# Kernel optimization log

Measured on AMD Instinct MI355X. Metric: run time of the kernel, lower is better.

Reference implementation:

```python
import jax, jax.numpy as jnp
import numpy as np

HASH = 1 << 12
EPS = 1e-5
_OFFS = [(dx, dy, dz) for dx in (-1, 0, 1) for dy in (-1, 0, 1) for dz in (-1, 0, 1)]
_KOFF = [k for k, o in enumerate(_OFFS) if o != (0, 0, 0)]  # 26 non-center taps
_CENTER = 13


def _hkey(c):
    c = c.astype(np.int64)
    return (c[:, 0] * HASH + c[:, 1]) * HASH + c[:, 2]


def _rand_coords(rng, n, R):
    idx = rng.choice(R ** 3, size=n, replace=False)
    return np.stack(np.unravel_index(idx, (R, R, R)), axis=1).astype(np.int64)


def _conv3_maps(coords):
    # ME kernel map for a 3x3x3 stride-1 conv (in coords == out coords):
    # per non-center tap, (gather_idx, scatter_idx) pairs found by hash lookup.
    n = coords.shape[0]
    keys = _hkey(coords)
    order = np.argsort(keys)
    skeys = keys[order]
    ins, outs = [], []
    for k in _KOFF:
        qk = _hkey(coords + np.asarray(_OFFS[k], np.int64))
        pos = np.clip(np.searchsorted(skeys, qk), 0, n - 1)
        valid = skeys[pos] == qk
        outs.append(np.nonzero(valid)[0].astype(np.int32))
        ins.append(order[pos[valid]].astype(np.int32))
    m = max(len(a) for a in ins)
    im = np.zeros((26, m), np.int32)    # pad gathers with row 0
    om = np.full((26, m), n, np.int32)  # pad scatters into scrap row n (dropped)
    for j in range(26):
        im[j, :len(ins[j])] = ins[j]
        om[j, :len(outs[j])] = outs[j]
    return np.stack([im, om])  # [2, 26, M]


def _children(coords):
    # generative transpose conv k=2 s=2 output coords, ordered o*n + i
    offs = np.array([[a, b, c] for a in (0, 1) for b in (0, 1) for c in (0, 1)], np.int64)
    return (2 * coords[None] + offs[:, None]).reshape(-1, 3)


def _union(ca, cb):
    # sparse-tensor addition domain: union of coordinate sets
    ka, kb = _hkey(ca), _hkey(cb)
    ku = np.unique(np.concatenate([ka, kb]))
    cu = np.stack([ku // (HASH * HASH), (ku // HASH) % HASH, ku % HASH], axis=1)
    return cu, np.searchsorted(ku, ka).astype(np.int32), np.searchsorted(ku, kb).astype(np.int32)


def _sconv3(x, W, m):
    # sparse 3^3 conv as gather-GEMM-scatter; center tap is a plain GEMM
    n = x.shape[0]
    acc = jnp.zeros((n + 1, W.shape[2]), x.dtype)
    for j, k in enumerate(_KOFF):
        acc = acc.at[m[1, j]].add(x[m[0, j]] @ W[k])
    return acc[:n] + x @ W[_CENTER]


def _bn_elu(x, p):
    # MinkowskiBatchNorm (training-mode batch stats over active voxels) + ELU
    mu = jnp.mean(x, axis=0)
    var = jnp.mean(jnp.square(x - mu), axis=0)
    return jax.nn.elu(p[0] * (x - mu) * jax.lax.rsqrt(var + EPS) + p[1])


def _up_block(x, Wt, Wc, m, pa, pb):
    # generative transpose conv (every voxel emits 8 children, order o*n+i) -> BN -> ELU -> conv3 -> BN -> ELU
    t = jnp.einsum('nc,ocd->ond', x, Wt).reshape(-1, Wt.shape[2])
    return _bn_elu(_sconv3(_bn_elu(t, pa), Wc, m), pb)


def setup_inputs() -> dict:
    rng = np.random.default_rng(0)
    N2, N1, N0 = 1200, 6000, 16000
    C2 = _rand_coords(rng, N2, 40)
    C1 = _rand_coords(rng, N1, 80)
    C0 = _rand_coords(rng, N0, 160)
    G2 = _children(C2)                       # coords after up_block_2 transpose conv
    U1, lat1_idx, up1_idx = _union(C1, G2)   # inputs[1] + x domain
    G1 = _children(U1)
    U0, lat0_idx, up0_idx = _union(C0, G1)   # inputs[0] + x domain

    key = jax.random.key(0)
    ks = list(jax.random.split(key, 32))
    kit = iter(ks)

    def w(shape, fan_in):
        return jax.random.normal(next(kit), shape, jnp.float32) * np.float32(1.0 / np.sqrt(fan_in))

    def bn(c):
        g = 1.0 + 0.1 * jax.random.normal(next(kit), (c,), jnp.float32)
        b = 0.1 * jax.random.normal(next(kit), (c,), jnp.float32)
        return jnp.stack([g, b])

    return dict(
        feats0=jax.random.normal(next(kit), (N0, 64), jnp.float32),
        feats1=jax.random.normal(next(kit), (N1, 128), jnp.float32),
        feats2=jax.random.normal(next(kit), (N2, 256), jnp.float32),
        w_out0=w((27, 64, 128), 27 * 64),
        w_out1=w((27, 128, 128), 27 * 128),
        w_out2=w((27, 256, 128), 27 * 256),
        wt2=w((8, 256, 128), 256),
        wu2=w((27, 128, 128), 27 * 128),
        wt1=w((8, 128, 64), 128),
        wu1=w((27, 64, 64), 27 * 64),
        bn_out0=bn(128), bn_out1=bn(128), bn_out2=bn(128),
        bn_up2a=bn(128), bn_up2b=bn(128),
        bn_up1a=bn(64), bn_up1b=bn(64),
        u1_base=jnp.zeros((U1.shape[0], 128), jnp.float32),
        u0_base=jnp.zeros((U0.shape[0], 64), jnp.float32),
        m_c2=jnp.asarray(_conv3_maps(C2)),
        m_g2=jnp.asarray(_conv3_maps(G2)),
        m_u1=jnp.asarray(_conv3_maps(U1)),
        m_g1=jnp.asarray(_conv3_maps(G1)),
        m_u0=jnp.asarray(_conv3_maps(U0)),
        lat1_idx=jnp.asarray(lat1_idx), up1_idx=jnp.asarray(up1_idx),
        lat0_idx=jnp.asarray(lat0_idx), up0_idx=jnp.asarray(up0_idx),
    )


def reference(feats0, feats1, feats2, w_out0, w_out1, w_out2, wt2, wu2, wt1, wu1,
              bn_out0, bn_out1, bn_out2, bn_up2a, bn_up2b, bn_up1a, bn_up1b,
              u1_base, u0_base, m_c2, m_g2, m_u1, m_g1, m_u0,
              lat1_idx, up1_idx, lat0_idx, up0_idx):
    # i = 2 (top)
    out2 = _bn_elu(_sconv3(feats2, w_out2, m_c2), bn_out2)
    t = _up_block(feats2, wt2, wu2, m_g2, bn_up2a, bn_up2b)
    # i = 1: sparse add over union of coords, then out/up blocks
    x1 = u1_base.at[lat1_idx].add(feats1).at[up1_idx].add(t)
    out1 = _bn_elu(_sconv3(x1, w_out1, m_u1), bn_out1)
    t = _up_block(x1, wt1, wu1, m_g1, bn_up1a, bn_up1b)
    # i = 0
    x0 = u0_base.at[lat0_idx].add(feats0).at[up0_idx].add(t)
    out0 = _bn_elu(_sconv3(x0, w_out0, m_u0), bn_out0)
    return out0, out1, out2
```

## Files before the change

kernel.cpp:

```cpp
#include <hip/hip_runtime.h>

typedef __bf16 bf16x8 __attribute__((ext_vector_type(8)));
typedef float  f32x4  __attribute__((ext_vector_type(4)));

__device__ __forceinline__ float b2f(unsigned short u) {
    union { unsigned int i; float f; } v; v.i = ((unsigned int)u) << 16; return v.f;
}
__device__ __forceinline__ unsigned short f2b(float f) {
    union { float f; unsigned int i; } v; v.f = f;
    unsigned int u = v.i;
    return (unsigned short)((u + 0x7fffu + ((u >> 16) & 1u)) >> 16);
}

__global__ void table_init(int* __restrict__ tab, int n)
{
    int idx = blockIdx.x * blockDim.x + threadIdx.x;
    if (idx >= n * 27) return;
    tab[idx] = ((idx % 27) == 13) ? (idx / 27) : n;
}

__global__ void table_fill(int* __restrict__ tab, const int* __restrict__ map, int M, int n)
{
    int tid = blockIdx.x * blockDim.x + threadIdx.x;
    if (tid >= 26 * M) return;
    int j = tid / M, q = tid - j * M;
    int om = map[(26 + j) * M + q];
    if (om < n) {
        int k = (j < 13) ? j : j + 1;
        tab[om * 27 + k] = map[j * M + q];
    }
}

__global__ void pack_w(const float* __restrict__ W, unsigned short* __restrict__ P,
                       int total, int log2Cout, int log2KC)
{
    int tid = blockIdx.x * blockDim.x + threadIdx.x;
    if (tid >= total) return;
    int jj   = tid & 7;
    int cout = (tid >> 3) & ((1 << log2Cout) - 1);
    int rest = tid >> (3 + log2Cout);
    int quad = rest & 3;
    int kj   = rest >> 2;
    int kc   = kj & ((1 << log2KC) - 1);
    int j    = kj >> log2KC;
    int Cin  = (1 << log2KC) * 32;
    int Cout = 1 << log2Cout;
    P[tid] = f2b(W[((size_t)j * Cin + kc * 32 + quad * 8 + jj) * Cout + cout]);
}

__global__ void cast_bf16(const float* __restrict__ X, unsigned short* __restrict__ Y, int nElem)
{
    int tid = blockIdx.x * blockDim.x + threadIdx.x;
    if (tid < nElem) Y[tid] = f2b(X[tid]);
}

template<int T, int KC, bool OUTBF16>
__global__ __launch_bounds__(256) void conv_mfma_st(
    const unsigned short* __restrict__ Xb, const unsigned short* __restrict__ P,
    const int* __restrict__ tab, void* __restrict__ OutV, int n, int nblk)
{
    constexpr int Cin = KC * 32, Cout = 64 * T;
    constexpr int STRIDE = KC * 32 + 8;
    constexpr int CHUNKS = KC * 4;
    constexpr int RPR = 256 / CHUNKS;
    __shared__ int tps[64 * 27];
    __shared__ unsigned short abuf[2][64 * STRIDE];

    const int t = threadIdx.x, lane = t & 63, wv = t >> 6;
    const int m = lane & 15, quad = lane >> 4;

    const int q = nblk >> 3, rr = nblk & 7;
    const int xcd = blockIdx.x & 7, pos = blockIdx.x >> 3;
    const int bswz = (xcd < rr) ? (xcd * (q + 1) + pos) : (rr * (q + 1) + (xcd - rr) * q + pos);
    const int r0 = bswz * 64;
    int rows = n - r0; if (rows > 64) rows = 64;

    for (int e = t; e < 64 * 27; e += 256)
        tps[e] = (e < rows * 27) ? tab[(size_t)r0 * 27 + e] : n;
    __syncthreads();

    const int sr = t / CHUNKS;
    const int sc = t % CHUNKS;

    f32x4 acc[4][T];
    #pragma unroll
    for (int rt = 0; rt < 4; rt++)
        #pragma unroll
        for (int c = 0; c < T; c++) acc[rt][c] = f32x4{0.f, 0.f, 0.f, 0.f};

    uint4 sreg[KC];

    #pragma unroll
    for (int rd = 0; rd < KC; rd++) {
        int r = rd * RPR + sr;
        int in = tps[r * 27];
        sreg[rd] = *reinterpret_cast<const uint4*>(Xb + (size_t)in * Cin + sc * 8);
    }
    #pragma unroll
    for (int rd = 0; rd < KC; rd++) {
        int r = rd * RPR + sr;
        *reinterpret_cast<uint4*>(&abuf[0][r * STRIDE + sc * 8]) = sreg[rd];
    }
    __syncthreads();

    for (int j = 0; j < 27; j++) {
        const int cur = j & 1;
        if (j + 1 < 27) {
            #pragma unroll
            for (int rd = 0; rd < KC; rd++) {
                int r = rd * RPR + sr;
                int in = tps[r * 27 + j + 1];
                sreg[rd] = *reinterpret_cast<const uint4*>(Xb + (size_t)in * Cin + sc * 8);
            }
        }
        #pragma unroll
        for (int kc = 0; kc < KC; kc++) {
            bf16x8 a[4];
            #pragma unroll
            for (int rt = 0; rt < 4; rt++)
                a[rt] = *reinterpret_cast<const bf16x8*>(&abuf[cur][(rt * 16 + m) * STRIDE + kc * 32 + quad * 8]);
            const unsigned short* bp = P + ((size_t)((j * KC + kc) * 4 + quad) * Cout + wv * (T * 16)) * 8;
            #pragma unroll
            for (int c = 0; c < T; c++) {
                bf16x8 b = *reinterpret_cast<const bf16x8*>(bp + (c * 16 + m) * 8);
                #pragma unroll
                for (int rt = 0; rt < 4; rt++)
                    acc[rt][c] = __builtin_amdgcn_mfma_f32_16x16x32_bf16(a[rt], b, acc[rt][c], 0, 0, 0);
            }
        }
        if (j + 1 < 27) {
            #pragma unroll
            for (int rd = 0; rd < KC; rd++) {
                int r = rd * RPR + sr;
                *reinterpret_cast<uint4*>(&abuf[cur ^ 1][r * STRIDE + sc * 8]) = sreg[rd];
            }
        }
        __syncthreads();
    }

    #pragma unroll
    for (int c = 0; c < T; c++) {
        int cout = (wv * T + c) * 16 + m;
        #pragma unroll
        for (int rt = 0; rt < 4; rt++) {
            #pragma unroll
            for (int reg = 0; reg < 4; reg++) {
                int r = rt * 16 + quad * 4 + reg;
                if (r < rows) {
                    size_t off = (size_t)(r0 + r) * Cout + cout;
                    if (OUTBF16) ((unsigned short*)OutV)[off] = f2b(acc[rt][c][reg]);
                    else         ((float*)OutV)[off] = acc[rt][c][reg];
                }
            }
        }
    }
}

template<int T, int RB, bool OUTBF16>
__global__ __launch_bounds__(256) void conv_mfma(
    const unsigned short* __restrict__ Xb, const unsigned short* __restrict__ P,
    const int* __restrict__ tab, void* __restrict__ OutV, int n, int Cin, int KC, int nblk)
{
    const int Cout = 64 * T;
    const int ROWS = RB * 16;
    __shared__ int tps[RB * 16 * 27];
    __shared__ int vld[27];
    const int t = threadIdx.x, lane = t & 63, wv = t >> 6;
    const int m = lane & 15, quad = lane >> 4;

    const int q = nblk >> 3, rr = nblk & 7;
    const int xcd = blockIdx.x & 7, pos = blockIdx.x >> 3;
    const int bswz = (xcd < rr) ? (xcd * (q + 1) + pos) : (rr * (q + 1) + (xcd - rr) * q + pos);
    const int r0 = bswz * ROWS;
    int rows = n - r0; if (rows > ROWS) rows = ROWS;

    for (int e = t; e < ROWS * 27; e += 256)
        tps[e] = (e < rows * 27) ? tab[(size_t)r0 * 27 + e] : n;
    __syncthreads();
    if constexpr (RB == 1) {
        if (t < 27) {
            int v = 0;
            for (int r = 0; r < 16; r++) v |= (tps[r * 27 + t] < n) ? 1 : 0;
            vld[t] = v;
        }
        __syncthreads();
    }

    f32x4 acc[RB][T];
    #pragma unroll
    for (int rt = 0; rt < RB; rt++)
        #pragma unroll
        for (int c = 0; c < T; c++) acc[rt][c] = f32x4{0.f, 0.f, 0.f, 0.f};

    const unsigned short* Xq = Xb + quad * 8;
    const unsigned short* Pq = P + ((size_t)quad * Cout + wv * (T * 16)) * 8;

    for (int j = 0; j < 27; j++) {
        if constexpr (RB == 1) {
            if (!vld[j]) continue;
        }
        int in[RB];
        #pragma unroll
        for (int rt = 0; rt < RB; rt++) in[rt] = tps[(rt * 16 + m) * 27 + j];
        for (int kc = 0; kc < KC; kc++) {
            bf16x8 a[RB];
            #pragma unroll
            for (int rt = 0; rt < RB; rt++)
                a[rt] = *reinterpret_cast<const bf16x8*>(Xq + (size_t)in[rt] * Cin + kc * 32);
            const unsigned short* bp = Pq + (size_t)((j * KC + kc) * 4) * Cout * 8;
            #pragma unroll
            for (int c = 0; c < T; c++) {
                bf16x8 b = *reinterpret_cast<const bf16x8*>(bp + (c * 16 + m) * 8);
                #pragma unroll
                for (int rt = 0; rt < RB; rt++)
                    acc[rt][c] = __builtin_amdgcn_mfma_f32_16x16x32_bf16(a[rt], b, acc[rt][c], 0, 0, 0);
            }
        }
    }

    #pragma unroll
    for (int c = 0; c < T; c++) {
        int cout = (wv * T + c) * 16 + m;
        #pragma unroll
        for (int rt = 0; rt < RB; rt++) {
            #pragma unroll
            for (int reg = 0; reg < 4; reg++) {
                int r = rt * 16 + quad * 4 + reg;
                if (r < rows) {
                    size_t off = (size_t)(r0 + r) * Cout + cout;
                    if (OUTBF16) ((unsigned short*)OutV)[off] = f2b(acc[rt][c][reg]);
                    else         ((float*)OutV)[off] = acc[rt][c][reg];
                }
            }
        }
    }
}

template<int KC, int T>
__global__ __launch_bounds__(256) void tconv_mfma(
    const unsigned short* __restrict__ Xb, const unsigned short* __restrict__ P,
    unsigned short* __restrict__ Out, int n)
{
    const int Cin = KC * 32, Cout = 64 * T;
    const int t = threadIdx.x, lane = t & 63, wv = t >> 6;
    const int m = lane & 15, quad = lane >> 4;
    const int r0 = blockIdx.x * 16;
    int rows = n - r0; if (rows > 16) rows = 16;

    bf16x8 a[KC];
    #pragma unroll
    for (int kc = 0; kc < KC; kc++) {
        a[kc] = bf16x8{};
        if (m < rows)
            a[kc] = *reinterpret_cast<const bf16x8*>(Xb + (size_t)(r0 + m) * Cin + kc * 32 + quad * 8);
    }

    for (int o = 0; o < 8; o++) {
        f32x4 acc[T];
        #pragma unroll
        for (int c = 0; c < T; c++) acc[c] = f32x4{0.f, 0.f, 0.f, 0.f};
        #pragma unroll
        for (int kc = 0; kc < KC; kc++) {
            const unsigned short* bp = P + ((size_t)((o * KC + kc) * 4 + quad) * Cout + wv * (T * 16)) * 8;
            #pragma unroll
            for (int c = 0; c < T; c++) {
                bf16x8 b = *reinterpret_cast<const bf16x8*>(bp + (c * 16 + m) * 8);
                acc[c] = __builtin_amdgcn_mfma_f32_16x16x32_bf16(a[kc], b, acc[c], 0, 0, 0);
            }
        }
        #pragma unroll
        for (int c = 0; c < T; c++) {
            int cout = (wv * T + c) * 16 + m;
            #pragma unroll
            for (int reg = 0; reg < 4; reg++) {
                int r = quad * 4 + reg;
                if (r < rows)
                    Out[((size_t)o * n + r0 + r) * Cout + cout] = f2b(acc[c][reg]);
            }
        }
    }
}

__global__ void scatter_add_f32(float* __restrict__ dst, const float* __restrict__ src,
                                const int* __restrict__ idx, long total, int C)
{
    long tid = (long)blockIdx.x * blockDim.x + threadIdx.x;
    if (tid >= total) return;
    long r = tid / C;
    int  c = (int)(tid - r * C);
    dst[(long)idx[r] * C + c] += src[tid];
}

__global__ void scatter_add_b16(float* __restrict__ dst, const unsigned short* __restrict__ src,
                                const int* __restrict__ idx, long total, int C)
{
    long tid = (long)blockIdx.x * blockDim.x + threadIdx.x;
    if (tid >= total) return;
    long r = tid / C;
    int  c = (int)(tid - r * C);
    dst[(long)idx[r] * C + c] += b2f(src[tid]);
}

template<bool BF16>
__global__ void bn_stats_k(const void* __restrict__ Xv, float* __restrict__ stats,
                           int n, int C, int rowsPerBlock)
{
    const int t = threadIdx.x;
    const int c = t & (C - 1);
    const int sub = t / C;
    const int nsub = 256 / C;
    int r0 = blockIdx.x * rowsPerBlock + sub;
    int r1 = blockIdx.x * rowsPerBlock + rowsPerBlock;
    if (r1 > n) r1 = n;
    float s = 0.f, ss = 0.f;
    for (int r = r0; r < r1; r += nsub) {
        float v = BF16 ? b2f(((const unsigned short*)Xv)[(long)r * C + c])
                       : ((const float*)Xv)[(long)r * C + c];
        s += v; ss += v * v;
    }
    __shared__ float bs[256];
    __shared__ float bq[256];
    bs[t] = s; bq[t] = ss;
    __syncthreads();
    if (sub == 0) {
        for (int k = 1; k < nsub; k++) { s += bs[k * C + c]; ss += bq[k * C + c]; }
        atomicAdd(&stats[c], s);
        atomicAdd(&stats[C + c], ss);
    }
}

template<bool BF16>
__global__ void bn_apply_k(void* __restrict__ Xv, const float* __restrict__ stats,
                           const float* __restrict__ gb, long total, int C, float invn)
{
    long tid = (long)blockIdx.x * blockDim.x + threadIdx.x;
    if (tid >= total) return;
    int c = (int)(tid & (C - 1));
    float mu  = stats[c] * invn;
    float var = stats[C + c] * invn - mu * mu;
    float sc  = gb[c] * rsqrtf(var + 1e-5f);
    float x   = BF16 ? b2f(((unsigned short*)Xv)[tid]) : ((float*)Xv)[tid];
    float v   = (x - mu) * sc + gb[C + c];
    v = (v > 0.f) ? v : expm1f(v);
    if (BF16) ((unsigned short*)Xv)[tid] = f2b(v);
    else      ((float*)Xv)[tid] = v;
}

extern "C" void kernel_launch(void* const* d_in, const int* in_sizes, int n_in,
                              void* d_out, int out_size, void* d_ws, size_t ws_size,
                              hipStream_t stream)
{
    const float* feats0  = (const float*)d_in[0];
    const float* feats1  = (const float*)d_in[1];
    const float* feats2  = (const float*)d_in[2];
    const float* w_out0  = (const float*)d_in[3];
    const float* w_out1  = (const float*)d_in[4];
    const float* w_out2  = (const float*)d_in[5];
    const float* wt2     = (const float*)d_in[6];
    const float* wu2     = (const float*)d_in[7];
    const float* wt1     = (const float*)d_in[8];
    const float* wu1     = (const float*)d_in[9];
    const float* bn_out0 = (const float*)d_in[10];
    const float* bn_out1 = (const float*)d_in[11];
    const float* bn_out2 = (const float*)d_in[12];
    const float* bn_up2a = (const float*)d_in[13];
    const float* bn_up2b = (const float*)d_in[14];
    const float* bn_up1a = (const float*)d_in[15];
    const float* bn_up1b = (const float*)d_in[16];
    const int* m_c2 = (const int*)d_in[19];
    const int* m_g2 = (const int*)d_in[20];
    const int* m_u1 = (const int*)d_in[21];
    const int* m_g1 = (const int*)d_in[22];
    const int* m_u0 = (const int*)d_in[23];
    const int* lat1 = (const int*)d_in[24];
    const int* up1  = (const int*)d_in[25];
    const int* lat0 = (const int*)d_in[26];
    const int* up0  = (const int*)d_in[27];

    const int N0  = in_sizes[0] / 64;
    const int N1  = in_sizes[1] / 128;
    const int N2  = in_sizes[2] / 256;
    const int U1  = in_sizes[17] / 128;
    const int U0  = in_sizes[18] / 64;
    const int G2n = in_sizes[25];
    const int G1n = in_sizes[27];
    const int Mc2 = in_sizes[19] / 52;
    const int Mg2 = in_sizes[20] / 52;
    const int Mu1 = in_sizes[21] / 52;
    const int Mg1 = in_sizes[22] / 52;
    const int Mu0 = in_sizes[23] / 52;

    float* out0 = (float*)d_out;
    float* out1 = out0 + (size_t)U0 * 128;
    float* out2 = out1 + (size_t)U1 * 128;

    char* wp = (char*)d_ws;
    auto alloc = [&](size_t bytes) -> char* {
        char* r = wp; wp += (bytes + 255) & ~(size_t)255; return r;
    };
    float*          x0   = (float*)alloc((size_t)U0 * 64 * 4);
    unsigned short* t1   = (unsigned short*)alloc((size_t)(G1n + 1) * 64 * 2);
    unsigned short* t1c  = (unsigned short*)alloc((size_t)(G1n + 1) * 64 * 2);
    unsigned short* t2   = (unsigned short*)alloc((size_t)(G2n + 1) * 128 * 2);
    unsigned short* t2c  = (unsigned short*)alloc((size_t)(G2n + 1) * 128 * 2);
    float*          x1   = (float*)alloc((size_t)U1 * 128 * 4);
    unsigned short* x1b  = (unsigned short*)alloc((size_t)(U1 + 1) * 128 * 2);
    unsigned short* x0b  = (unsigned short*)alloc((size_t)(U0 + 1) * 64 * 2);
    unsigned short* f2bb = (unsigned short*)alloc((size_t)(N2 + 1) * 256 * 2);
    unsigned short* pc2  = (unsigned short*)alloc((size_t)27 * 256 * 128 * 2);
    unsigned short* pt2  = (unsigned short*)alloc((size_t)8  * 256 * 128 * 2);
    unsigned short* pg2  = (unsigned short*)alloc((size_t)27 * 128 * 128 * 2);
    unsigned short* pu1  = (unsigned short*)alloc((size_t)27 * 128 * 128 * 2);
    unsigned short* pt1  = (unsigned short*)alloc((size_t)8  * 128 * 64  * 2);
    unsigned short* pg1  = (unsigned short*)alloc((size_t)27 * 64  * 64  * 2);
    unsigned short* pu0  = (unsigned short*)alloc((size_t)27 * 64  * 128 * 2);
    int maxSmall = (U1 > G2n) ? U1 : G2n;
    int*   smallTab = (int*)alloc((size_t)maxSmall * 27 * 4);
    float* stats    = (float*)alloc(1024);
    int* tab_g1 = (int*)x0;
    int* tab_u0 = (int*)t1;

    hipMemsetAsync(f2bb + (size_t)N2  * 256, 0, 256 * 2, stream);
    hipMemsetAsync(t2   + (size_t)G2n * 128, 0, 128 * 2, stream);
    hipMemsetAsync(x1b  + (size_t)U1  * 128, 0, 128 * 2, stream);
    hipMemsetAsync(t1   + (size_t)G1n * 64,  0, 64  * 2, stream);
    hipMemsetAsync(x0b  + (size_t)U0  * 64,  0, 64  * 2, stream);

    auto packW = [&](const float* W, unsigned short* P, int taps, int l2co, int l2kc) {
        int total = taps * ((1 << l2kc) * 32) * (1 << l2co);
        pack_w<<<dim3((total + 255) / 256), dim3(256), 0, stream>>>(W, P, total, l2co, l2kc);
    };
    auto cast = [&](const float* X, unsigned short* Y, long nElem) {
        cast_bf16<<<dim3((int)((nElem + 255) / 256)), dim3(256), 0, stream>>>(X, Y, (int)nElem);
    };
    auto buildTab = [&](int* tab, const int* map, int M, int n) {
        table_init<<<dim3((n * 27 + 255) / 256), dim3(256), 0, stream>>>(tab, n);
        table_fill<<<dim3((26 * M + 255) / 256), dim3(256), 0, stream>>>(tab, map, M, n);
    };
    auto conv = [&](const unsigned short* Xb, const unsigned short* P, const int* tab,
                    void* Out, int n, int Cin, int Cout, bool outbf16) {
        int KC = Cin / 32;
        if (n >= 12000) {
            int nblk = (n + 63) / 64;
            dim3 g(nblk), b(256);
            if (Cout == 128 && KC == 2) {
                if (outbf16) conv_mfma_st<2, 2, true ><<<g, b, 0, stream>>>(Xb, P, tab, Out, n, nblk);
                else         conv_mfma_st<2, 2, false><<<g, b, 0, stream>>>(Xb, P, tab, Out, n, nblk);
                return;
            }
            if (Cout == 64 && KC == 2) {
                if (outbf16) conv_mfma_st<1, 2, true ><<<g, b, 0, stream>>>(Xb, P, tab, Out, n, nblk);
                else         conv_mfma_st<1, 2, false><<<g, b, 0, stream>>>(Xb, P, tab, Out, n, nblk);
                return;
            }
            if (Cout == 128 && KC == 4) {
                if (outbf16) conv_mfma_st<2, 4, true ><<<g, b, 0, stream>>>(Xb, P, tab, Out, n, nblk);
                else         conv_mfma_st<2, 4, false><<<g, b, 0, stream>>>(Xb, P, tab, Out, n, nblk);
                return;
            }
        }
        int RB = (n >= 12000) ? 2 : 1;
        int nblk = (n + RB * 16 - 1) / (RB * 16);
        dim3 g(nblk), b(256);
        #define CONV_CASE(T_, RB_)                                                                        \
            if (Cout == 64 * T_ && RB == RB_) {                                                           \
                if (outbf16) conv_mfma<T_, RB_, true ><<<g, b, 0, stream>>>(Xb, P, tab, Out, n, Cin, KC, nblk); \
                else         conv_mfma<T_, RB_, false><<<g, b, 0, stream>>>(Xb, P, tab, Out, n, Cin, KC, nblk); \
                return;                                                                                   \
            }
        CONV_CASE(2, 2) CONV_CASE(2, 1)
        CONV_CASE(1, 2) CONV_CASE(1, 1)
        #undef CONV_CASE
    };
    auto bnelu = [&](void* X, const float* gb, int n, int C, bool bf16) {
        hipMemsetAsync(stats, 0, 2 * C * sizeof(float), stream);
        const int rpb = 512;
        long total = (long)n * C;
        if (bf16) {
            bn_stats_k<true ><<<dim3((n + rpb - 1) / rpb), dim3(256), 0, stream>>>(X, stats, n, C, rpb);
            bn_apply_k<true ><<<dim3((int)((total + 255) / 256)), dim3(256), 0, stream>>>(X, stats, gb, total, C, 1.0f / n);
        } else {
            bn_stats_k<false><<<dim3((n + rpb - 1) / rpb), dim3(256), 0, stream>>>(X, stats, n, C, rpb);
            bn_apply_k<false><<<dim3((int)((total + 255) / 256)), dim3(256), 0, stream>>>(X, stats, gb, total, C, 1.0f / n);
        }
    };

    cast(feats2, f2bb, (long)N2 * 256);
    packW(w_out2, pc2, 27, 7, 3);
    packW(wt2,    pt2,  8, 7, 3);
    packW(wu2,    pg2, 27, 7, 2);
    packW(w_out1, pu1, 27, 7, 2);
    packW(wt1,    pt1,  8, 6, 2);
    packW(wu1,    pg1, 27, 6, 1);
    packW(w_out0, pu0, 27, 7, 1);

    buildTab(smallTab, m_c2, Mc2, N2);
    conv(f2bb, pc2, smallTab, out2, N2, 256, 128, false);
    bnelu(out2, bn_out2, N2, 128, false);
    tconv_mfma<8, 2><<<dim3((N2 + 15) / 16), dim3(256), 0, stream>>>(f2bb, pt2, t2, N2);
    bnelu(t2, bn_up2a, G2n, 128, true);
    buildTab(smallTab, m_g2, Mg2, G2n);
    conv(t2, pg2, smallTab, t2c, G2n, 128, 128, true);
    bnelu(t2c, bn_up2b, G2n, 128, true);

    hipMemsetAsync(x1, 0, (size_t)U1 * 128 * sizeof(float), stream);
    {
        long tot = (long)N1 * 128;
        scatter_add_f32<<<dim3((int)((tot + 255) / 256)), dim3(256), 0, stream>>>(x1, feats1, lat1, tot, 128);
        tot = (long)G2n * 128;
        scatter_add_b16<<<dim3((int)((tot + 255) / 256)), dim3(256), 0, stream>>>(x1, t2c, up1, tot, 128);
    }
    cast(x1, x1b, (long)U1 * 128);
    buildTab(smallTab, m_u1, Mu1, U1);
    conv(x1b, pu1, smallTab, out1, U1, 128, 128, false);
    bnelu(out1, bn_out1, U1, 128, false);
    tconv_mfma<4, 1><<<dim3((U1 + 15) / 16), dim3(256), 0, stream>>>(x1b, pt1, t1, U1);
    bnelu(t1, bn_up1a, G1n, 64, true);
    buildTab(tab_g1, m_g1, Mg1, G1n);
    conv(t1, pg1, tab_g1, t1c, G1n, 64, 64, true);
    bnelu(t1c, bn_up1b, G1n, 64, true);

    hipMemsetAsync(x0, 0, (size_t)U0 * 64 * sizeof(float), stream);
    {
        long tot = (long)N0 * 64;
        scatter_add_f32<<<dim3((int)((tot + 255) / 256)), dim3(256), 0, stream>>>(x0, feats0, lat0, tot, 64);
        tot = (long)G1n * 64;
        scatter_add_b16<<<dim3((int)((tot + 255) / 256)), dim3(256), 0, stream>>>(x0, t1c, up0, tot, 64);
    }
    buildTab(tab_u0, m_u0, Mu0, U0);
    cast(x0, x0b, (long)U0 * 64);
    conv(x0b, pu0, tab_u0, out0, U0, 64, 128, false);
    bnelu(out0, bn_out0, U0, 128, false);
}
```

Baseline: 1.111 ms.

## Fuse BN statistics into conv epilogue and enlarge row tiles for big convs

The streaming MFMA conv kernel now accumulates per-channel sum and sum-of-squares in its epilogue, using wave shuffles and atomics. This lets the out1, up1b and out0 layers skip the separate bn_stats pass and its re-read of the conv output. The row tile is now a template parameter, and convs with n ≥ 40000 and Cin=64 use 128-row blocks. The gather prefetch is also moved so loads for tap j+2 are issued right after tap j+1's data is written to LDS. Fused stats rely on these layers always taking the conv_mfma_st path, since the fallback kernel ignores the stats pointer; atomics and the larger tile add contention and register pressure.

Result: no change. 1.114 ms (+0.3%).

```diff
diff --git a/kernel.cpp b/kernel.cpp
--- a/kernel.cpp
+++ b/kernel.cpp
@@ -54,17 +54,20 @@
     if (tid < nElem) Y[tid] = f2b(X[tid]);
 }
 
-template<int T, int KC, bool OUTBF16>
+template<int T, int KC, int RT, bool OUTBF16>
 __global__ __launch_bounds__(256) void conv_mfma_st(
     const unsigned short* __restrict__ Xb, const unsigned short* __restrict__ P,
-    const int* __restrict__ tab, void* __restrict__ OutV, int n, int nblk)
+    const int* __restrict__ tab, void* __restrict__ OutV, float* __restrict__ St,
+    int n, int nblk)
 {
     constexpr int Cin = KC * 32, Cout = 64 * T;
+    constexpr int ROWS = RT * 16;
     constexpr int STRIDE = KC * 32 + 8;
     constexpr int CHUNKS = KC * 4;
     constexpr int RPR = 256 / CHUNKS;
-    __shared__ int tps[64 * 27];
-    __shared__ unsigned short abuf[2][64 * STRIDE];
+    constexpr int NRD = ROWS / RPR;
+    __shared__ int tps[ROWS * 27];
+    __shared__ unsigned short abuf[2][ROWS * STRIDE];
 
     const int t = threadIdx.x, lane = t & 63, wv = t >> 6;
     const int m = lane & 15, quad = lane >> 4;
@@ -72,67 +75,65 @@
     const int q = nblk >> 3, rr = nblk & 7;
     const int xcd = blockIdx.x & 7, pos = blockIdx.x >> 3;
     const int bswz = (xcd < rr) ? (xcd * (q + 1) + pos) : (rr * (q + 1) + (xcd - rr) * q + pos);
-    const int r0 = bswz * 64;
-    int rows = n - r0; if (rows > 64) rows = 64;
-
-    for (int e = t; e < 64 * 27; e += 256)
+    const int r0 = bswz * ROWS;
+    int rows = n - r0; if (rows > ROWS) rows = ROWS;
+
+    for (int e = t; e < ROWS * 27; e += 256)
         tps[e] = (e < rows * 27) ? tab[(size_t)r0 * 27 + e] : n;
     __syncthreads();
 
-    const int sr = t / CHUNKS;
-    const int sc = t % CHUNKS;
-
-    f32x4 acc[4][T];
-    #pragma unroll
-    for (int rt = 0; rt < 4; rt++)
+    const int sr = t / CHUNKS, sc = t % CHUNKS;
+
+    f32x4 acc[RT][T];
+    #pragma unroll
+    for (int rt = 0; rt < RT; rt++)
         #pragma unroll
         for (int c = 0; c < T; c++) acc[rt][c] = f32x4{0.f, 0.f, 0.f, 0.f};
 
-    uint4 sreg[KC];
-
-    #pragma unroll
-    for (int rd = 0; rd < KC; rd++) {
-        int r = rd * RPR + sr;
-        int in = tps[r * 27];
+    uint4 sreg[NRD];
+
+    #pragma unroll
+    for (int rd = 0; rd < NRD; rd++) {
+        int in = tps[(rd * RPR + sr) * 27 + 0];
         sreg[rd] = *reinterpret_cast<const uint4*>(Xb + (size_t)in * Cin + sc * 8);
     }
     #pragma unroll
-    for (int rd = 0; rd < KC; rd++) {
-        int r = rd * RPR + sr;
-        *reinterpret_cast<uint4*>(&abuf[0][r * STRIDE + sc * 8]) = sreg[rd];
+    for (int rd = 0; rd < NRD; rd++)
+        *reinterpret_cast<uint4*>(&abuf[0][(rd * RPR + sr) * STRIDE + sc * 8]) = sreg[rd];
+    #pragma unroll
+    for (int rd = 0; rd < NRD; rd++) {
+        int in = tps[(rd * RPR + sr) * 27 + 1];
+        sreg[rd] = *reinterpret_cast<const uint4*>(Xb + (size_t)in * Cin + sc * 8);
     }
     __syncthreads();
 
     for (int j = 0; j < 27; j++) {
         const int cur = j & 1;
-        if (j + 1 < 27) {
-            #pragma unroll
-            for (int rd = 0; rd < KC; rd++) {
-                int r = rd * RPR + sr;
-                int in = tps[r * 27 + j + 1];
-                sreg[rd] = *reinterpret_cast<const uint4*>(Xb + (size_t)in * Cin + sc * 8);
-            }
-        }
         #pragma unroll
         for (int kc = 0; kc < KC; kc++) {
-            bf16x8 a[4];
-            #pragma unroll
-            for (int rt = 0; rt < 4; rt++)
+            bf16x8 a[RT];
+            #pragma unroll
+            for (int rt = 0; rt < RT; rt++)
                 a[rt] = *reinterpret_cast<const bf16x8*>(&abuf[cur][(rt * 16 + m) * STRIDE + kc * 32 + quad * 8]);
             const unsigned short* bp = P + ((size_t)((j * KC + kc) * 4 + quad) * Cout + wv * (T * 16)) * 8;
             #pragma unroll
             for (int c = 0; c < T; c++) {
                 bf16x8 b = *reinterpret_cast<const bf16x8*>(bp + (c * 16 + m) * 8);
                 #pragma unroll
-                for (int rt = 0; rt < 4; rt++)
+                for (int rt = 0; rt < RT; rt++)
                     acc[rt][c] = __builtin_amdgcn_mfma_f32_16x16x32_bf16(a[rt], b, acc[rt][c], 0, 0, 0);
             }
         }
         if (j + 1 < 27) {
             #pragma unroll
-            for (int rd = 0; rd < KC; rd++) {
-                int r = rd * RPR + sr;
-                *reinterpret_cast<uint4*>(&abuf[cur ^ 1][r * STRIDE + sc * 8]) = sreg[rd];
+            for (int rd = 0; rd < NRD; rd++)
+                *reinterpret_cast<uint4*>(&abuf[cur ^ 1][(rd * RPR + sr) * STRIDE + sc * 8]) = sreg[rd];
+            if (j + 2 < 27) {
+                #pragma unroll
+                for (int rd = 0; rd < NRD; rd++) {
+                    int in = tps[(rd * RPR + sr) * 27 + j + 2];
+                    sreg[rd] = *reinterpret_cast<const uint4*>(Xb + (size_t)in * Cin + sc * 8);
+                }
             }
         }
         __syncthreads();
@@ -140,17 +141,33 @@
 
     #pragma unroll
     for (int c = 0; c < T; c++) {
-        int cout = (wv * T + c) * 16 + m;
-        #pragma unroll
-        for (int rt = 0; rt < 4; rt++) {
+        const int cout = (wv * T + c) * 16 + m;
+        float s = 0.f, ss = 0.f;
+        #pragma unroll
+        for (int rt = 0; rt < RT; rt++) {
             #pragma unroll
             for (int reg = 0; reg < 4; reg++) {
                 int r = rt * 16 + quad * 4 + reg;
                 if (r < rows) {
+                    float v = acc[rt][c][reg];
                     size_t off = (size_t)(r0 + r) * Cout + cout;
-                    if (OUTBF16) ((unsigned short*)OutV)[off] = f2b(acc[rt][c][reg]);
-                    else         ((float*)OutV)[off] = acc[rt][c][reg];
+                    if (OUTBF16) {
+                        unsigned short h = f2b(v);
+                        ((unsigned short*)OutV)[off] = h;
+                        v = b2f(h);
+                    } else {
+                        ((float*)OutV)[off] = v;
+                    }
+                    s += v; ss += v * v;
                 }
+            }
+        }
+        if (St) {
+            s  += __shfl_xor(s, 16);  ss += __shfl_xor(ss, 16);
+            s  += __shfl_xor(s, 32);  ss += __shfl_xor(ss, 32);
+            if (quad == 0) {
+                atomicAdd(&St[cout], s);
+                atomicAdd(&St[Cout + cout], ss);
             }
         }
     }
@@ -438,24 +455,36 @@
         table_fill<<<dim3((26 * M + 255) / 256), dim3(256), 0, stream>>>(tab, map, M, n);
     };
     auto conv = [&](const unsigned short* Xb, const unsigned short* P, const int* tab,
-                    void* Out, int n, int Cin, int Cout, bool outbf16) {
+                    void* Out, int n, int Cin, int Cout, bool outbf16, float* st) {
         int KC = Cin / 32;
+        if (n >= 40000 && KC == 2) {
+            int nblk = (n + 127) / 128;
+            dim3 g(nblk), b(256);
+            if (Cout == 128) {
+                if (outbf16) conv_mfma_st<2, 2, 8, true ><<<g, b, 0, stream>>>(Xb, P, tab, Out, st, n, nblk);
+                else         conv_mfma_st<2, 2, 8, false><<<g, b, 0, stream>>>(Xb, P, tab, Out, st, n, nblk);
+            } else {
+                if (outbf16) conv_mfma_st<1, 2, 8, true ><<<g, b, 0, stream>>>(Xb, P, tab, Out, st, n, nblk);
+                else         conv_mfma_st<1, 2, 8, false><<<g, b, 0, stream>>>(Xb, P, tab, Out, st, n, nblk);
+            }
+            return;
+        }
         if (n >= 12000) {
             int nblk = (n + 63) / 64;
             dim3 g(nblk), b(256);
+            if (Cout == 128 && KC == 4) {
+                if (outbf16) conv_mfma_st<2, 4, 4, true ><<<g, b, 0, stream>>>(Xb, P, tab, Out, st, n, nblk);
+                else         conv_mfma_st<2, 4, 4, false><<<g, b, 0, stream>>>(Xb, P, tab, Out, st, n, nblk);
+                return;
+            }
             if (Cout == 128 && KC == 2) {
-                if (outbf16) conv_mfma_st<2, 2, true ><<<g, b, 0, stream>>>(Xb, P, tab, Out, n, nblk);
-                else         conv_mfma_st<2, 2, false><<<g, b, 0, stream>>>(Xb, P, tab, Out, n, nblk);
+                if (outbf16) conv_mfma_st<2, 2, 4, true ><<<g, b, 0, stream>>>(Xb, P, tab, Out, st, n, nblk);
+                else         conv_mfma_st<2, 2, 4, false><<<g, b, 0, stream>>>(Xb, P, tab, Out, st, n, nblk);
                 return;
             }
             if (Cout == 64 && KC == 2) {
-                if (outbf16) conv_mfma_st<1, 2, true ><<<g, b, 0, stream>>>(Xb, P, tab, Out, n, nblk);
-                else         conv_mfma_st<1, 2, false><<<g, b, 0, stream>>>(Xb, P, tab, Out, n, nblk);
-                return;
-            }
-            if (Cout == 128 && KC == 4) {
-                if (outbf16) conv_mfma_st<2, 4, true ><<<g, b, 0, stream>>>(Xb, P, tab, Out, n, nblk);
-                else         conv_mfma_st<2, 4, false><<<g, b, 0, stream>>>(Xb, P, tab, Out, n, nblk);
+                if (outbf16) conv_mfma_st<1, 2, 4, true ><<<g, b, 0, stream>>>(Xb, P, tab, Out, st, n, nblk);
+                else         conv_mfma_st<1, 2, 4, false><<<g, b, 0, stream>>>(Xb, P, tab, Out, st, n, nblk);
                 return;
             }
         }
@@ -472,17 +501,17 @@
         CONV_CASE(1, 2) CONV_CASE(1, 1)
         #undef CONV_CASE
     };
+    auto bnapply = [&](void* X, const float* gb, int n, int C, bool bf16) {
+        long total = (long)n * C;
+        if (bf16) bn_apply_k<true ><<<dim3((int)((total + 255) / 256)), dim3(256), 0, stream>>>(X, stats, gb, total, C, 1.0f / n);
+        else      bn_apply_k<false><<<dim3((int)((total + 255) / 256)), dim3(256), 0, stream>>>(X, stats, gb, total, C, 1.0f / n);
+    };
     auto bnelu = [&](void* X, const float* gb, int n, int C, bool bf16) {
         hipMemsetAsync(stats, 0, 2 * C * sizeof(float), stream);
         const int rpb = 512;
-        long total = (long)n * C;
-        if (bf16) {
-            bn_stats_k<true ><<<dim3((n + rpb - 1) / rpb), dim3(256), 0, stream>>>(X, stats, n, C, rpb);
-            bn_apply_k<true ><<<dim3((int)((total + 255) / 256)), dim3(256), 0, stream>>>(X, stats, gb, total, C, 1.0f / n);
-        } else {
-            bn_stats_k<false><<<dim3((n + rpb - 1) / rpb), dim3(256), 0, stream>>>(X, stats, n, C, rpb);
-            bn_apply_k<false><<<dim3((int)((total + 255) / 256)), dim3(256), 0, stream>>>(X, stats, gb, total, C, 1.0f / n);
-        }
+        if (bf16) bn_stats_k<true ><<<dim3((n + rpb - 1) / rpb), dim3(256), 0, stream>>>(X, stats, n, C, rpb);
+        else      bn_stats_k<false><<<dim3((n + rpb - 1) / rpb), dim3(256), 0, stream>>>(X, stats, n, C, rpb);
+        bnapply(X, gb, n, C, bf16);
     };
 
     cast(feats2, f2bb, (long)N2 * 256);
@@ -495,12 +524,12 @@
     packW(w_out0, pu0, 27, 7, 1);
 
     buildTab(smallTab, m_c2, Mc2, N2);
-    conv(f2bb, pc2, smallTab, out2, N2, 256, 128, false);
+    conv(f2bb, pc2, smallTab, out2, N2, 256, 128, false, nullptr);
     bnelu(out2, bn_out2, N2, 128, false);
     tconv_mfma<8, 2><<<dim3((N2 + 15) / 16), dim3(256), 0, stream>>>(f2bb, pt2, t2, N2);
     bnelu(t2, bn_up2a, G2n, 128, true);
     buildTab(smallTab, m_g2, Mg2, G2n);
-    conv(t2, pg2, smallTab, t2c, G2n, 128, 128, true);
+    conv(t2, pg2, smallTab, t2c, G2n, 128, 128, true, nullptr);
     bnelu(t2c, bn_up2b, G2n, 128, true);
 
     hipMemsetAsync(x1, 0, (size_t)U1 * 128 * sizeof(float), stream);
@@ -512,13 +541,15 @@
     }
     cast(x1, x1b, (long)U1 * 128);
     buildTab(smallTab, m_u1, Mu1, U1);
-    conv(x1b, pu1, smallTab, out1, U1, 128, 128, false);
-    bnelu(out1, bn_out1, U1, 128, false);
+    hipMemsetAsync(stats, 0, 2 * 128 * sizeof(float), stream);
+    conv(x1b, pu1, smallTab, out1, U1, 128, 128, false, stats);
+    bnapply(out1, bn_out1, U1, 128, false);
     tconv_mfma<4, 1><<<dim3((U1 + 15) / 16), dim3(256), 0, stream>>>(x1b, pt1, t1, U1);
     bnelu(t1, bn_up1a, G1n, 64, true);
     buildTab(tab_g1, m_g1, Mg1, G1n);
-    conv(t1, pg1, tab_g1, t1c, G1n, 64, 64, true);
-    bnelu(t1c, bn_up1b, G1n, 64, true);
+    hipMemsetAsync(stats, 0, 2 * 64 * sizeof(float), stream);
+    conv(t1, pg1, tab_g1, t1c, G1n, 64, 64, true, stats);
+    bnapply(t1c, bn_up1b, G1n, 64, true);
 
     hipMemsetAsync(x0, 0, (size_t)U0 * 64 * sizeof(float), stream);
     {
@@ -529,6 +560,7 @@
     }
     buildTab(tab_u0, m_u0, Mu0, U0);
     cast(x0, x0b, (long)U0 * 64);
-    conv(x0b, pu0, tab_u0, out0, U0, 64, 128, false);
-    bnelu(out0, bn_out0, U0, 128, false);
-}
+    hipMemsetAsync(stats, 0, 2 * 128 * sizeof(float), stream);
+    conv(x0b, pu0, tab_u0, out0, U0, 64, 128, false, stats);
+    bnapply(out0, bn_out0, U0, 128, false);
+}
```

## Fuse BatchNorm statistics accumulation into the large sparse-conv epilogue

Applied to the files above, without the earlier changes.

The 64-row-tile conv kernel now sums each output channel and its square in registers, reduces them across the wave with shuffles, and adds them atomically into a stats buffer. For the three large convs (out1, up1b, out0) this replaces the separate bn_stats pass over the conv output with a memset plus the fused epilogue, avoiding one full read of each output. For bf16 outputs the stats use the rounded values to match what is stored. Stats are only filled on the n >= 12000 path, so a smaller layer would get empty stats, and per-block atomics on a few hundred addresses add some contention.

Measured after the change: 992.9 us. 10.7% less time.

```diff
diff --git a/kernel.cpp b/kernel.cpp
--- a/kernel.cpp
+++ b/kernel.cpp
@@ -57,7 +57,8 @@
 template<int T, int KC, bool OUTBF16>
 __global__ __launch_bounds__(256) void conv_mfma_st(
     const unsigned short* __restrict__ Xb, const unsigned short* __restrict__ P,
-    const int* __restrict__ tab, void* __restrict__ OutV, int n, int nblk)
+    const int* __restrict__ tab, void* __restrict__ OutV, float* __restrict__ St,
+    int n, int nblk)
 {
     constexpr int Cin = KC * 32, Cout = 64 * T;
     constexpr int STRIDE = KC * 32 + 8;
@@ -140,17 +141,33 @@
 
     #pragma unroll
     for (int c = 0; c < T; c++) {
-        int cout = (wv * T + c) * 16 + m;
+        const int cout = (wv * T + c) * 16 + m;
+        float s = 0.f, ss = 0.f;
         #pragma unroll
         for (int rt = 0; rt < 4; rt++) {
             #pragma unroll
             for (int reg = 0; reg < 4; reg++) {
                 int r = rt * 16 + quad * 4 + reg;
                 if (r < rows) {
+                    float v = acc[rt][c][reg];
                     size_t off = (size_t)(r0 + r) * Cout + cout;
-                    if (OUTBF16) ((unsigned short*)OutV)[off] = f2b(acc[rt][c][reg]);
-                    else         ((float*)OutV)[off] = acc[rt][c][reg];
+                    if (OUTBF16) {
+                        unsigned short h = f2b(v);
+                        ((unsigned short*)OutV)[off] = h;
+                        v = b2f(h);
+                    } else {
+                        ((float*)OutV)[off] = v;
+                    }
+                    s += v; ss += v * v;
                 }
+            }
+        }
+        if (St) {
+            s  += __shfl_xor(s, 16);  ss += __shfl_xor(ss, 16);
+            s  += __shfl_xor(s, 32);  ss += __shfl_xor(ss, 32);
+            if (quad == 0) {
+                atomicAdd(&St[cout], s);
+                atomicAdd(&St[Cout + cout], ss);
             }
         }
     }
@@ -438,24 +455,24 @@
         table_fill<<<dim3((26 * M + 255) / 256), dim3(256), 0, stream>>>(tab, map, M, n);
     };
     auto conv = [&](const unsigned short* Xb, const unsigned short* P, const int* tab,
-                    void* Out, int n, int Cin, int Cout, bool outbf16) {
+                    void* Out, int n, int Cin, int Cout, bool outbf16, float* st) {
         int KC = Cin / 32;
         if (n >= 12000) {
             int nblk = (n + 63) / 64;
             dim3 g(nblk), b(256);
             if (Cout == 128 && KC == 2) {
-                if (outbf16) conv_mfma_st<2, 2, true ><<<g, b, 0, stream>>>(Xb, P, tab, Out, n, nblk);
-                else         conv_mfma_st<2, 2, false><<<g, b, 0, stream>>>(Xb, P, tab, Out, n, nblk);
+                if (outbf16) conv_mfma_st<2, 2, true ><<<g, b, 0, stream>>>(Xb, P, tab, Out, st, n, nblk);
+                else         conv_mfma_st<2, 2, false><<<g, b, 0, stream>>>(Xb, P, tab, Out, st, n, nblk);
                 return;
             }
             if (Cout == 64 && KC == 2) {
-                if (outbf16) conv_mfma_st<1, 2, true ><<<g, b, 0, stream>>>(Xb, P, tab, Out, n, nblk);
-                else         conv_mfma_st<1, 2, false><<<g, b, 0, stream>>>(Xb, P, tab, Out, n, nblk);
+                if (outbf16) conv_mfma_st<1, 2, true ><<<g, b, 0, stream>>>(Xb, P, tab, Out, st, n, nblk);
+                else         conv_mfma_st<1, 2, false><<<g, b, 0, stream>>>(Xb, P, tab, Out, st, n, nblk);
                 return;
             }
             if (Cout == 128 && KC == 4) {
-                if (outbf16) conv_mfma_st<2, 4, true ><<<g, b, 0, stream>>>(Xb, P, tab, Out, n, nblk);
-                else         conv_mfma_st<2, 4, false><<<g, b, 0, stream>>>(Xb, P, tab, Out, n, nblk);
+                if (outbf16) conv_mfma_st<2, 4, true ><<<g, b, 0, stream>>>(Xb, P, tab, Out, st, n, nblk);
+                else         conv_mfma_st<2, 4, false><<<g, b, 0, stream>>>(Xb, P, tab, Out, st, n, nblk);
                 return;
             }
         }
@@ -472,17 +489,17 @@
         CONV_CASE(1, 2) CONV_CASE(1, 1)
         #undef CONV_CASE
     };
+    auto bnapply = [&](void* X, const float* gb, int n, int C, bool bf16) {
+        long total = (long)n * C;
+        if (bf16) bn_apply_k<true ><<<dim3((int)((total + 255) / 256)), dim3(256), 0, stream>>>(X, stats, gb, total, C, 1.0f / n);
+        else      bn_apply_k<false><<<dim3((int)((total + 255) / 256)), dim3(256), 0, stream>>>(X, stats, gb, total, C, 1.0f / n);
+    };
     auto bnelu = [&](void* X, const float* gb, int n, int C, bool bf16) {
         hipMemsetAsync(stats, 0, 2 * C * sizeof(float), stream);
         const int rpb = 512;
-        long total = (long)n * C;
-        if (bf16) {
-            bn_stats_k<true ><<<dim3((n + rpb - 1) / rpb), dim3(256), 0, stream>>>(X, stats, n, C, rpb);
-            bn_apply_k<true ><<<dim3((int)((total + 255) / 256)), dim3(256), 0, stream>>>(X, stats, gb, total, C, 1.0f / n);
-        } else {
-            bn_stats_k<false><<<dim3((n + rpb - 1) / rpb), dim3(256), 0, stream>>>(X, stats, n, C, rpb);
-            bn_apply_k<false><<<dim3((int)((total + 255) / 256)), dim3(256), 0, stream>>>(X, stats, gb, total, C, 1.0f / n);
-        }
+        if (bf16) bn_stats_k<true ><<<dim3((n + rpb - 1) / rpb), dim3(256), 0, stream>>>(X, stats, n, C, rpb);
+        else      bn_stats_k<false><<<dim3((n + rpb - 1) / rpb), dim3(256), 0, stream>>>(X, stats, n, C, rpb);
+        bnapply(X, gb, n, C, bf16);
     };
 
     cast(feats2, f2bb, (long)N2 * 256);
@@ -495,12 +512,12 @@
     packW(w_out0, pu0, 27, 7, 1);
 
     buildTab(smallTab, m_c2, Mc2, N2);
-    conv(f2bb, pc2, smallTab, out2, N2, 256, 128, false);
+    conv(f2bb, pc2, smallTab, out2, N2, 256, 128, false, nullptr);
     bnelu(out2, bn_out2, N2, 128, false);
     tconv_mfma<8, 2><<<dim3((N2 + 15) / 16), dim3(256), 0, stream>>>(f2bb, pt2, t2, N2);
     bnelu(t2, bn_up2a, G2n, 128, true);
     buildTab(smallTab, m_g2, Mg2, G2n);
-    conv(t2, pg2, smallTab, t2c, G2n, 128, 128, true);
+    conv(t2, pg2, smallTab, t2c, G2n, 128, 128, true, nullptr);
     bnelu(t2c, bn_up2b, G2n, 128, true);
 
     hipMemsetAsync(x1, 0, (size_t)U1 * 128 * sizeof(float), stream);
@@ -512,13 +529,15 @@
     }
     cast(x1, x1b, (long)U1 * 128);
     buildTab(smallTab, m_u1, Mu1, U1);
-    conv(x1b, pu1, smallTab, out1, U1, 128, 128, false);
-    bnelu(out1, bn_out1, U1, 128, false);
+    hipMemsetAsync(stats, 0, 2 * 128 * sizeof(float), stream);
+    conv(x1b, pu1, smallTab, out1, U1, 128, 128, false, stats);
+    bnapply(out1, bn_out1, U1, 128, false);
     tconv_mfma<4, 1><<<dim3((U1 + 15) / 16), dim3(256), 0, stream>>>(x1b, pt1, t1, U1);
     bnelu(t1, bn_up1a, G1n, 64, true);
     buildTab(tab_g1, m_g1, Mg1, G1n);
-    conv(t1, pg1, tab_g1, t1c, G1n, 64, 64, true);
-    bnelu(t1c, bn_up1b, G1n, 64, true);
+    hipMemsetAsync(stats, 0, 2 * 64 * sizeof(float), stream);
+    conv(t1, pg1, tab_g1, t1c, G1n, 64, 64, true, stats);
+    bnapply(t1c, bn_up1b, G1n, 64, true);
 
     hipMemsetAsync(x0, 0, (size_t)U0 * 64 * sizeof(float), stream);
     {
@@ -529,6 +548,7 @@
     }
     buildTab(tab_u0, m_u0, Mu0, U0);
     cast(x0, x0b, (long)U0 * 64);
-    conv(x0b, pu0, tab_u0, out0, U0, 64, 128, false);
-    bnelu(out0, bn_out0, U0, 128, false);
-}
+    hipMemsetAsync(stats, 0, 2 * 128 * sizeof(float), stream);
+    conv(x0b, pu0, tab_u0, out0, U0, 64, 128, false, stats);
+    bnapply(out0, bn_out0, U0, 128, false);
+}
```
